# Optimization experiments

Measured on AMD Instinct MI355X. Metric: run time of the kernel, lower is better.

## Reference

```python
import jax, jax.numpy as jnp
import numpy as np

B, N, K, C, CE, H = 2, 2048, 48, 128, 128, 128
IN = 2 * C + CE  # 384
AGG_SCALE = 30.0
LN_EPS = 1e-5


def setup_inputs() -> dict:
    key = jax.random.key(0)
    ks = jax.random.split(key, 12)
    inp = {
        "node_h": jax.random.normal(ks[0], (B, N, C), jnp.float32),
        "edge_h": jax.random.normal(ks[1], (B, N, K, CE), jnp.float32),
        "edge_index": jax.random.randint(ks[2], (B, N, K), 0, N, jnp.int64),
        # message MLP: Linear(IN,H) GELU Linear(H,H) GELU Linear(H,C)
        "W1": jax.random.normal(ks[3], (IN, H), jnp.float32) / np.sqrt(IN),
        "b1": jnp.zeros((H,), jnp.float32),
        "W2": jax.random.normal(ks[4], (H, H), jnp.float32) / np.sqrt(H),
        "b2": jnp.zeros((H,), jnp.float32),
        "W3": jax.random.normal(ks[5], (H, C), jnp.float32) / np.sqrt(H),
        "b3": jnp.zeros((C,), jnp.float32),
        "Wu": jax.random.normal(ks[6], (C, C), jnp.float32) / np.sqrt(C),
        "bu": jnp.zeros((C,), jnp.float32),
        "ln_g": jnp.ones((C,), jnp.float32),
        "ln_b": jnp.zeros((C,), jnp.float32),
    }
    return inp


def _layer_norm(x, g, b):
    mu = jnp.mean(x, axis=-1, keepdims=True)
    var = jnp.var(x, axis=-1, keepdims=True)
    return (x - mu) * jax.lax.rsqrt(var + LN_EPS) * g + b


def _gelu(x):
    return jax.nn.gelu(x, approximate=False)  # torch nn.GELU default (erf)


def reference(node_h, edge_h, edge_index, W1, b1, W2, b2, W3, b3, Wu, bu, ln_g, ln_b):
    b, n, k = edge_index.shape
    c = node_h.shape[-1]
    # gather neighbor node features: (B,N,K,C)
    node_j = jnp.take_along_axis(
        node_h, edge_index.reshape(b, n * k)[..., None], axis=1
    ).reshape(b, n, k, c)
    node_i = jnp.broadcast_to(node_h[:, :, None, :], (b, n, k, c))
    edge_packed = jnp.concatenate([node_i, node_j, edge_h], axis=-1)  # (B,N,K,IN)
    # message MLP
    h = _gelu(edge_packed @ W1 + b1)
    h = _gelu(h @ W2 + b2)
    messages = (h @ W3 + b3).sum(axis=-2) / AGG_SCALE  # (B,N,C)
    # dropout is identity in eval mode
    updated_nodes = _layer_norm(node_h + messages, ln_g, ln_b)
    node_updates = updated_nodes @ Wu + bu
    out = _layer_norm(node_h + node_updates, ln_g, ln_b)
    return out
```

## Files before the change

kernel.cpp:

```cpp
#include <hip/hip_runtime.h>
#include <hip/hip_bf16.h>
#include <math.h>

#define Bn   2
#define Nn   2048
#define Kn   48
#define Cn   128
#define G2   16

#define SIG(r) ((((r) ^ ((r) >> 2))) & 7)

typedef short bf16x8 __attribute__((ext_vector_type(8)));
typedef float f32x4  __attribute__((ext_vector_type(4)));

#if __has_builtin(__builtin_amdgcn_cvt_pk_bf16_f32)
#define HAS_PK 1
#endif

__device__ __forceinline__ short f2bf(float f) {
  union { float f; unsigned u; } v; v.f = f;
  unsigned r = v.u + 0x7fffu + ((v.u >> 16) & 1u);
  return (short)(r >> 16);
}

__device__ __forceinline__ unsigned pk2(float a, float b) {
#ifdef HAS_PK
  auto p = __builtin_amdgcn_cvt_pk_bf16_f32(a, b);
  return __builtin_bit_cast(unsigned, p);
#else
  return (unsigned)(unsigned short)f2bf(a) | ((unsigned)(unsigned short)f2bf(b) << 16);
#endif
}

__device__ __forceinline__ float gelu_f(float x) {
  float z = x * (-2.3021991f - 0.10294200f * x * x);
  float e = __builtin_amdgcn_exp2f(z);
  return x * __builtin_amdgcn_rcpf(1.0f + e);
}

__global__ void pack_weights(const float* __restrict__ W1,
                             const float* __restrict__ W2,
                             const float* __restrict__ W3,
                             const float* __restrict__ Wu,
                             short* __restrict__ ws) {
  int tid = blockIdx.x * blockDim.x + threadIdx.x;
  if (tid >= 192 * 64) return;
  int lane = tid & 63;
  int tile = tid >> 6;
  const float* W; short* dst;
  if (tile < 32)       { W = W1;         dst = ws; }
  else if (tile < 96)  { W = W1 + 16384; dst = ws + 16384; tile -= 32; }
  else if (tile < 128) { W = W2;         dst = ws + 49152; tile -= 96; }
  else if (tile < 160) { W = W3;         dst = ws + 65536; tile -= 128; }
  else                 { W = Wu;         dst = ws + 81920; tile -= 160; }
  int kt = tile >> 3, nt = tile & 7;
  int n  = nt * 16 + (lane & 15);
  int k0 = kt * 32 + (lane >> 4) * 8;
  union { short s[8]; bf16x8 v; } u8;
#pragma unroll
  for (int j = 0; j < 8; j++) u8.s[j] = f2bf(W[(k0 + j) * 128 + n]);
  *reinterpret_cast<bf16x8*>(dst + (tile << 9) + lane * 8) = u8.v;
}

__global__ __launch_bounds__(256, 6)
void node_update_kernel(const float* __restrict__ node_h,
                        const float* __restrict__ edge_h,
                        const int*   __restrict__ edge_index,
                        const short* __restrict__ wpack,
                        const float* __restrict__ b1,
                        const float* __restrict__ b2,
                        float* __restrict__ hs_out) {
  __shared__ __align__(16) char smem[24576];
  short* Xs  = (short*)smem;
  short* H1s = (short*)(smem + 12288);

  const int tid  = threadIdx.x;
  const int blk  = blockIdx.x;
  const int bb   = blk >> 11;
  const int lane = tid & 63;
  const int wave = tid >> 6;
  const int lr   = lane & 15;
  const int lq   = lane >> 4;

  const short* W1i = wpack;
  const short* W1e = wpack + 16384;
  const short* W2p = wpack + 49152;

  const int w  = tid & 31;
  const int rr = tid >> 5;
  int idxv[6];
  if (w < 16) {
#pragma unroll
    for (int k = 0; k < 6; k++)
      idxv[k] = edge_index[blk * Kn + rr + k * 8];
  }

  f32x4 accY[2] = {};
  {
    bf16x8 avk[4] = {{0}, {0}, {0}, {0}};
    if (lr == 0) {
      const float* p = node_h + (size_t)blk * Cn;
#pragma unroll
      for (int kt = 0; kt < 4; kt++) {
        float4 a0 = *reinterpret_cast<const float4*>(p + kt * 32 + lq * 8);
        float4 a1 = *reinterpret_cast<const float4*>(p + kt * 32 + lq * 8 + 4);
        union { unsigned u[4]; bf16x8 v; } q;
        q.u[0] = pk2(a0.x, a0.y); q.u[1] = pk2(a0.z, a0.w);
        q.u[2] = pk2(a1.x, a1.y); q.u[3] = pk2(a1.z, a1.w);
        avk[kt] = q.v;
      }
    }
#pragma unroll
    for (int kt = 0; kt < 4; kt++) {
      bf16x8 bv0 = *reinterpret_cast<const bf16x8*>(W1i + ((kt * 8 + wave * 2 + 0) << 9) + lane * 8);
      bf16x8 bv1 = *reinterpret_cast<const bf16x8*>(W1i + ((kt * 8 + wave * 2 + 1) << 9) + lane * 8);
      accY[0] = __builtin_amdgcn_mfma_f32_16x16x32_bf16(avk[kt], bv0, accY[0], 0, 0, 0);
      accY[1] = __builtin_amdgcn_mfma_f32_16x16x32_bf16(avk[kt], bv1, accY[1], 0, 0, 0);
    }
  }

#pragma unroll
  for (int k = 0; k < 6; k++) {
    int r = rr + k * 8;
    const float* src = (w < 16)
        ? node_h + (size_t)(bb * Nn + idxv[k]) * Cn + w * 8
        : edge_h + ((size_t)blk * Kn + r) * Cn + (w - 16) * 8;
    float4 v0 = *reinterpret_cast<const float4*>(src);
    float4 v1 = *reinterpret_cast<const float4*>(src + 4);
    uint4 p;
    p.x = pk2(v0.x, v0.y); p.y = pk2(v0.z, v0.w);
    p.z = pk2(v1.x, v1.y); p.w = pk2(v1.z, v1.w);
    *reinterpret_cast<uint4*>(&Xs[r * 256 + ((w ^ SIG(r)) << 3)]) = p;
  }
  __syncthreads();

  const int s0 = SIG(lr);
  f32x4 acc[3][2] = {};
#pragma unroll
  for (int kt = 0; kt < 8; kt++) {
    bf16x8 bf0 = *reinterpret_cast<const bf16x8*>(W1e + ((kt * 8 + wave * 2 + 0) << 9) + lane * 8);
    bf16x8 bf1 = *reinterpret_cast<const bf16x8*>(W1e + ((kt * 8 + wave * 2 + 1) << 9) + lane * 8);
    int swA = (((kt * 4 + lq) ^ s0) << 3);
    int swB = swA ^ (4 << 3);
    bf16x8 a0 = *reinterpret_cast<const bf16x8*>(&Xs[(0  + lr) * 256 + swA]);
    bf16x8 a1 = *reinterpret_cast<const bf16x8*>(&Xs[(16 + lr) * 256 + swB]);
    bf16x8 a2 = *reinterpret_cast<const bf16x8*>(&Xs[(32 + lr) * 256 + swA]);
    acc[0][0] = __builtin_amdgcn_mfma_f32_16x16x32_bf16(a0, bf0, acc[0][0], 0, 0, 0);
    acc[0][1] = __builtin_amdgcn_mfma_f32_16x16x32_bf16(a0, bf1, acc[0][1], 0, 0, 0);
    acc[1][0] = __builtin_amdgcn_mfma_f32_16x16x32_bf16(a1, bf0, acc[1][0], 0, 0, 0);
    acc[1][1] = __builtin_amdgcn_mfma_f32_16x16x32_bf16(a1, bf1, acc[1][1], 0, 0, 0);
    acc[2][0] = __builtin_amdgcn_mfma_f32_16x16x32_bf16(a2, bf0, acc[2][0], 0, 0, 0);
    acc[2][1] = __builtin_amdgcn_mfma_f32_16x16x32_bf16(a2, bf1, acc[2][1], 0, 0, 0);
  }
  __syncthreads();

  const int s5 = (lq * 5) & 7;
#pragma unroll
  for (int j = 0; j < 2; j++) {
    int col = (wave * 2 + j) * 16 + lr;
    float yi = __shfl(accY[j][0], lr) + b1[col];
    int cl = col & 7;
#pragma unroll
    for (int mt = 0; mt < 3; mt++) {
      int r0 = mt * 16 + lq * 4;
      int gs = (col >> 3) ^ s5 ^ ((mt & 1) << 2);
      float g0 = gelu_f(acc[mt][j][0] + yi);
      float g1 = gelu_f(acc[mt][j][1] + yi);
      float g2 = gelu_f(acc[mt][j][2] + yi);
      float g3 = gelu_f(acc[mt][j][3] + yi);
      unsigned p01 = pk2(g0, g1), p23 = pk2(g2, g3);
      H1s[(r0 + 0) * 128 + ((gs ^ 0) << 3) + cl] = (short)(p01 & 0xffff);
      H1s[(r0 + 1) * 128 + ((gs ^ 1) << 3) + cl] = (short)(p01 >> 16);
      H1s[(r0 + 2) * 128 + ((gs ^ 2) << 3) + cl] = (short)(p23 & 0xffff);
      H1s[(r0 + 3) * 128 + ((gs ^ 3) << 3) + cl] = (short)(p23 >> 16);
    }
  }
  __syncthreads();

  f32x4 acc2[3][2] = {};
#pragma unroll
  for (int kt = 0; kt < 4; kt++) {
    bf16x8 bf0 = *reinterpret_cast<const bf16x8*>(W2p + ((kt * 8 + wave * 2 + 0) << 9) + lane * 8);
    bf16x8 bf1 = *reinterpret_cast<const bf16x8*>(W2p + ((kt * 8 + wave * 2 + 1) << 9) + lane * 8);
    int swA = (((kt * 4 + lq) ^ s0) << 3);
    int swB = swA ^ (4 << 3);
    bf16x8 a0 = *reinterpret_cast<const bf16x8*>(&H1s[(0  + lr) * 128 + swA]);
    bf16x8 a1 = *reinterpret_cast<const bf16x8*>(&H1s[(16 + lr) * 128 + swB]);
    bf16x8 a2 = *reinterpret_cast<const bf16x8*>(&H1s[(32 + lr) * 128 + swA]);
    acc2[0][0] = __builtin_amdgcn_mfma_f32_16x16x32_bf16(a0, bf0, acc2[0][0], 0, 0, 0);
    acc2[0][1] = __builtin_amdgcn_mfma_f32_16x16x32_bf16(a0, bf1, acc2[0][1], 0, 0, 0);
    acc2[1][0] = __builtin_amdgcn_mfma_f32_16x16x32_bf16(a1, bf0, acc2[1][0], 0, 0, 0);
    acc2[1][1] = __builtin_amdgcn_mfma_f32_16x16x32_bf16(a1, bf1, acc2[1][1], 0, 0, 0);
    acc2[2][0] = __builtin_amdgcn_mfma_f32_16x16x32_bf16(a2, bf0, acc2[2][0], 0, 0, 0);
    acc2[2][1] = __builtin_amdgcn_mfma_f32_16x16x32_bf16(a2, bf1, acc2[2][1], 0, 0, 0);
  }
#pragma unroll
  for (int j = 0; j < 2; j++) {
    int col = (wave * 2 + j) * 16 + lr;
    float bias = b2[col];
    float s = 0.f;
#pragma unroll
    for (int mt = 0; mt < 3; mt++)
#pragma unroll
      for (int r = 0; r < 4; r++) s += gelu_f(acc2[mt][j][r] + bias);
    s += __shfl_xor(s, 16);
    s += __shfl_xor(s, 32);
    if (lq == 0) hs_out[(size_t)blk * Cn + col] = s;
  }
}

__global__ __launch_bounds__(256, 4)
void tail_kernel(const float* __restrict__ node_h,
                 const short* __restrict__ wpack,
                 const float* __restrict__ b3,
                 const float* __restrict__ bu,
                 const float* __restrict__ ln_g,
                 const float* __restrict__ ln_b,
                 float* __restrict__ out) {
  __shared__ __align__(16) char sm2[24832];
  short* hsB = (short*)sm2;
  float* nhr = (float*)(sm2 + 4096);
  float* xs  = (float*)(sm2 + 12288);
  short* usB = (short*)(sm2 + 20736);

  const int tid  = threadIdx.x;
  const int lane = tid & 63;
  const int wave = tid >> 6;
  const int lr   = lane & 15;
  const int lq   = lane >> 4;
  const int n0   = blockIdx.x * G2;

  const short* W3p = wpack + 65536;
  const short* Wup = wpack + 81920;

  {
    int row = tid >> 4, seg = tid & 15;
    const float* p = node_h + (size_t)(n0 + row) * Cn + seg * 8;
    float4 a0 = *reinterpret_cast<const float4*>(p);
    float4 a1 = *reinterpret_cast<const float4*>(p + 4);
    *reinterpret_cast<float4*>(&nhr[row * 128 + seg * 8])     = a0;
    *reinterpret_cast<float4*>(&nhr[row * 128 + seg * 8 + 4]) = a1;
    const float* q = out + (size_t)(n0 + row) * Cn + seg * 8;
    float4 c0 = *reinterpret_cast<const float4*>(q);
    float4 c1 = *reinterpret_cast<const float4*>(q + 4);
    uint4 pk;
    pk.x = pk2(c0.x, c0.y); pk.y = pk2(c0.z, c0.w);
    pk.z = pk2(c1.x, c1.y); pk.w = pk2(c1.z, c1.w);
    *reinterpret_cast<uint4*>(&hsB[row * 128 + ((seg ^ (row & 7)) << 3)]) = pk;
  }
  __syncthreads();

  f32x4 am[2] = {};
#pragma unroll
  for (int kt = 0; kt < 4; kt++) {
    bf16x8 av = *reinterpret_cast<const bf16x8*>(&hsB[lr * 128 + (((kt * 4 + lq) ^ (lr & 7)) << 3)]);
    bf16x8 bv0 = *reinterpret_cast<const bf16x8*>(W3p + ((kt * 8 + wave * 2 + 0) << 9) + lane * 8);
    bf16x8 bv1 = *reinterpret_cast<const bf16x8*>(W3p + ((kt * 8 + wave * 2 + 1) << 9) + lane * 8);
    am[0] = __builtin_amdgcn_mfma_f32_16x16x32_bf16(av, bv0, am[0], 0, 0, 0);
    am[1] = __builtin_amdgcn_mfma_f32_16x16x32_bf16(av, bv1, am[1], 0, 0, 0);
  }
#pragma unroll
  for (int j = 0; j < 2; j++) {
    int col = (wave * 2 + j) * 16 + lr;
    float bb = 48.0f * b3[col];
#pragma unroll
    for (int r = 0; r < 4; r++) {
      int row = lq * 4 + r;
      xs[row * 132 + col] = nhr[row * 128 + col] + (am[j][r] + bb) * (1.0f / 30.0f);
    }
  }
  __syncthreads();

  const float lg1 = ln_g[lane],      lb1v = ln_b[lane];
  const float lg2 = ln_g[lane + 64], lb2v = ln_b[lane + 64];
#pragma unroll
  for (int s = 0; s < 4; s++) {
    int row = wave * 4 + s;
    float v1 = xs[row * 132 + lane];
    float v2 = xs[row * 132 + lane + 64];
    float s1 = v1 + v2, s2 = v1 * v1 + v2 * v2;
#pragma unroll
    for (int off = 32; off >= 1; off >>= 1) {
      s1 += __shfl_xor(s1, off);
      s2 += __shfl_xor(s2, off);
    }
    float mu = s1 * (1.f / 128.f);
    float var = s2 * (1.f / 128.f) - mu * mu;
    float rstd = rsqrtf(var + 1e-5f);
    unsigned u12 = pk2((v1 - mu) * rstd * lg1 + lb1v,
                       (v2 - mu) * rstd * lg2 + lb2v);
    int sw = (row & 7);
    usB[row * 128 + (((lane >> 3) ^ sw) << 3) + (lane & 7)]       = (short)(u12 & 0xffff);
    usB[row * 128 + ((((lane >> 3) + 8) ^ sw) << 3) + (lane & 7)] = (short)(u12 >> 16);
  }
  __syncthreads();

  f32x4 au[2] = {};
#pragma unroll
  for (int kt = 0; kt < 4; kt++) {
    bf16x8 av = *reinterpret_cast<const bf16x8*>(&usB[lr * 128 + (((kt * 4 + lq) ^ (lr & 7)) << 3)]);
    bf16x8 bv0 = *reinterpret_cast<const bf16x8*>(Wup + ((kt * 8 + wave * 2 + 0) << 9) + lane * 8);
    bf16x8 bv1 = *reinterpret_cast<const bf16x8*>(Wup + ((kt * 8 + wave * 2 + 1) << 9) + lane * 8);
    au[0] = __builtin_amdgcn_mfma_f32_16x16x32_bf16(av, bv0, au[0], 0, 0, 0);
    au[1] = __builtin_amdgcn_mfma_f32_16x16x32_bf16(av, bv1, au[1], 0, 0, 0);
  }
  __syncthreads();
#pragma unroll
  for (int j = 0; j < 2; j++) {
    int col = (wave * 2 + j) * 16 + lr;
    float bb = bu[col];
#pragma unroll
    for (int r = 0; r < 4; r++) {
      int row = lq * 4 + r;
      xs[row * 132 + col] = nhr[row * 128 + col] + au[j][r] + bb;
    }
  }
  __syncthreads();

#pragma unroll
  for (int s = 0; s < 4; s++) {
    int row = wave * 4 + s;
    float v1 = xs[row * 132 + lane];
    float v2 = xs[row * 132 + lane + 64];
    float s1 = v1 + v2, s2 = v1 * v1 + v2 * v2;
#pragma unroll
    for (int off = 32; off >= 1; off >>= 1) {
      s1 += __shfl_xor(s1, off);
      s2 += __shfl_xor(s2, off);
    }
    float mu = s1 * (1.f / 128.f);
    float var = s2 * (1.f / 128.f) - mu * mu;
    float rstd = rsqrtf(var + 1e-5f);
    out[(size_t)(n0 + row) * Cn + lane]      = (v1 - mu) * rstd * lg1 + lb1v;
    out[(size_t)(n0 + row) * Cn + lane + 64] = (v2 - mu) * rstd * lg2 + lb2v;
  }
}

extern "C" void kernel_launch(void* const* d_in, const int* in_sizes, int n_in,
                              void* d_out, int out_size, void* d_ws, size_t ws_size,
                              hipStream_t stream) {
  const float* node_h     = (const float*)d_in[0];
  const float* edge_h     = (const float*)d_in[1];
  const int*   edge_index = (const int*)  d_in[2];
  const float* W1 = (const float*)d_in[3];
  const float* b1 = (const float*)d_in[4];
  const float* W2 = (const float*)d_in[5];
  const float* b2 = (const float*)d_in[6];
  const float* W3 = (const float*)d_in[7];
  const float* b3 = (const float*)d_in[8];
  const float* Wu = (const float*)d_in[9];
  const float* bu = (const float*)d_in[10];
  const float* ln_g = (const float*)d_in[11];
  const float* ln_b = (const float*)d_in[12];
  float* out   = (float*)d_out;
  short* wpack = (short*)d_ws;

  pack_weights<<<48, 256, 0, stream>>>(W1, W2, W3, Wu, wpack);
  node_update_kernel<<<Bn * Nn, 256, 0, stream>>>(
      node_h, edge_h, edge_index, wpack, b1, b2, out);
  tail_kernel<<<(Bn * Nn) / G2, 256, 0, stream>>>(
      node_h, wpack, b3, bu, ln_g, ln_b, out);
}
```

Before: 208.5 us.

## Process two nodes per block in node update kernel to amortize weight loads

Each block of the node update kernel now handles two nodes (96 edge rows) rather than one, so every packed weight fragment loaded from global memory feeds twice as many MFMAs. The edge indices and the self-node features are staged in shared memory first. The X buffer and the first-layer hidden buffer now share one larger shared region, and launch bounds drop from 6 to 3 blocks per CU. In exchange there are more accumulator registers per thread, fewer resident waves to hide gather latency, and half as many blocks in the grid.

```diff
diff --git a/kernel.cpp b/kernel.cpp
--- a/kernel.cpp
+++ b/kernel.cpp
@@ -6,6 +6,7 @@
 #define Nn   2048
 #define Kn   48
 #define Cn   128
+#define NB   2
 #define G2   16
 
 #define SIG(r) ((((r) ^ ((r) >> 2))) & 7)
@@ -62,7 +63,7 @@
   *reinterpret_cast<bf16x8*>(dst + (tile << 9) + lane * 8) = u8.v;
 }
 
-__global__ __launch_bounds__(256, 6)
+__global__ __launch_bounds__(256, 3)
 void node_update_kernel(const float* __restrict__ node_h,
                         const float* __restrict__ edge_h,
                         const int*   __restrict__ edge_index,
@@ -70,13 +71,16 @@
                         const float* __restrict__ b1,
                         const float* __restrict__ b2,
                         float* __restrict__ hs_out) {
-  __shared__ __align__(16) char smem[24576];
-  short* Xs  = (short*)smem;
-  short* H1s = (short*)(smem + 12288);
+  __shared__ __align__(16) char smem[50048];
+  short* Xs    = (short*)smem;
+  short* H1s   = (short*)smem;
+  short* nhb   = (short*)(smem + 49152);
+  int*   idx_s = (int*)  (smem + 49664);
 
   const int tid  = threadIdx.x;
-  const int blk  = blockIdx.x;
-  const int bb   = blk >> 11;
+  const int blk2 = blockIdx.x;
+  const int n0   = blk2 * NB;
+  const int bb   = blk2 >> 10;
   const int lane = tid & 63;
   const int wave = tid >> 6;
   const int lr   = lane & 15;
@@ -86,71 +90,55 @@
   const short* W1e = wpack + 16384;
   const short* W2p = wpack + 49152;
 
-  const int w  = tid & 31;
-  const int rr = tid >> 5;
-  int idxv[6];
-  if (w < 16) {
-#pragma unroll
-    for (int k = 0; k < 6; k++)
-      idxv[k] = edge_index[blk * Kn + rr + k * 8];
+  nhb[tid] = f2bf(node_h[(size_t)n0 * Cn + tid]);
+  if (tid < 96) idx_s[tid] = edge_index[blk2 * (NB * Kn) + tid];
+  __syncthreads();
+
+  {
+    const int w  = tid & 31;
+    const int rr = tid >> 5;
+#pragma unroll
+    for (int k = 0; k < 12; k++) {
+      int r = rr + k * 8;
+      const float* src = (w < 16)
+          ? node_h + (size_t)(bb * Nn + idx_s[r]) * Cn + w * 8
+          : edge_h + (size_t)(blk2 * (NB * Kn) + r) * Cn + (w - 16) * 8;
+      float4 v0 = *reinterpret_cast<const float4*>(src);
+      float4 v1 = *reinterpret_cast<const float4*>(src + 4);
+      uint4 p;
+      p.x = pk2(v0.x, v0.y); p.y = pk2(v0.z, v0.w);
+      p.z = pk2(v1.x, v1.y); p.w = pk2(v1.z, v1.w);
+      *reinterpret_cast<uint4*>(&Xs[r * 256 + ((w ^ SIG(r)) << 3)]) = p;
+    }
   }
 
   f32x4 accY[2] = {};
-  {
-    bf16x8 avk[4] = {{0}, {0}, {0}, {0}};
-    if (lr == 0) {
-      const float* p = node_h + (size_t)blk * Cn;
-#pragma unroll
-      for (int kt = 0; kt < 4; kt++) {
-        float4 a0 = *reinterpret_cast<const float4*>(p + kt * 32 + lq * 8);
-        float4 a1 = *reinterpret_cast<const float4*>(p + kt * 32 + lq * 8 + 4);
-        union { unsigned u[4]; bf16x8 v; } q;
-        q.u[0] = pk2(a0.x, a0.y); q.u[1] = pk2(a0.z, a0.w);
-        q.u[2] = pk2(a1.x, a1.y); q.u[3] = pk2(a1.z, a1.w);
-        avk[kt] = q.v;
-      }
-    }
-#pragma unroll
-    for (int kt = 0; kt < 4; kt++) {
-      bf16x8 bv0 = *reinterpret_cast<const bf16x8*>(W1i + ((kt * 8 + wave * 2 + 0) << 9) + lane * 8);
-      bf16x8 bv1 = *reinterpret_cast<const bf16x8*>(W1i + ((kt * 8 + wave * 2 + 1) << 9) + lane * 8);
-      accY[0] = __builtin_amdgcn_mfma_f32_16x16x32_bf16(avk[kt], bv0, accY[0], 0, 0, 0);
-      accY[1] = __builtin_amdgcn_mfma_f32_16x16x32_bf16(avk[kt], bv1, accY[1], 0, 0, 0);
-    }
-  }
-
-#pragma unroll
-  for (int k = 0; k < 6; k++) {
-    int r = rr + k * 8;
-    const float* src = (w < 16)
-        ? node_h + (size_t)(bb * Nn + idxv[k]) * Cn + w * 8
-        : edge_h + ((size_t)blk * Kn + r) * Cn + (w - 16) * 8;
-    float4 v0 = *reinterpret_cast<const float4*>(src);
-    float4 v1 = *reinterpret_cast<const float4*>(src + 4);
-    uint4 p;
-    p.x = pk2(v0.x, v0.y); p.y = pk2(v0.z, v0.w);
-    p.z = pk2(v1.x, v1.y); p.w = pk2(v1.z, v1.w);
-    *reinterpret_cast<uint4*>(&Xs[r * 256 + ((w ^ SIG(r)) << 3)]) = p;
+#pragma unroll
+  for (int kt = 0; kt < 4; kt++) {
+    bf16x8 av = {};
+    if (lr < 2) av = *reinterpret_cast<const bf16x8*>(&nhb[lr * 128 + kt * 32 + lq * 8]);
+    bf16x8 bv0 = *reinterpret_cast<const bf16x8*>(W1i + ((kt * 8 + wave * 2 + 0) << 9) + lane * 8);
+    bf16x8 bv1 = *reinterpret_cast<const bf16x8*>(W1i + ((kt * 8 + wave * 2 + 1) << 9) + lane * 8);
+    accY[0] = __builtin_amdgcn_mfma_f32_16x16x32_bf16(av, bv0, accY[0], 0, 0, 0);
+    accY[1] = __builtin_amdgcn_mfma_f32_16x16x32_bf16(av, bv1, accY[1], 0, 0, 0);
   }
   __syncthreads();
 
   const int s0 = SIG(lr);
-  f32x4 acc[3][2] = {};
+  f32x4 acc[6][2] = {};
 #pragma unroll
   for (int kt = 0; kt < 8; kt++) {
     bf16x8 bf0 = *reinterpret_cast<const bf16x8*>(W1e + ((kt * 8 + wave * 2 + 0) << 9) + lane * 8);
     bf16x8 bf1 = *reinterpret_cast<const bf16x8*>(W1e + ((kt * 8 + wave * 2 + 1) << 9) + lane * 8);
     int swA = (((kt * 4 + lq) ^ s0) << 3);
     int swB = swA ^ (4 << 3);
-    bf16x8 a0 = *reinterpret_cast<const bf16x8*>(&Xs[(0  + lr) * 256 + swA]);
-    bf16x8 a1 = *reinterpret_cast<const bf16x8*>(&Xs[(16 + lr) * 256 + swB]);
-    bf16x8 a2 = *reinterpret_cast<const bf16x8*>(&Xs[(32 + lr) * 256 + swA]);
-    acc[0][0] = __builtin_amdgcn_mfma_f32_16x16x32_bf16(a0, bf0, acc[0][0], 0, 0, 0);
-    acc[0][1] = __builtin_amdgcn_mfma_f32_16x16x32_bf16(a0, bf1, acc[0][1], 0, 0, 0);
-    acc[1][0] = __builtin_amdgcn_mfma_f32_16x16x32_bf16(a1, bf0, acc[1][0], 0, 0, 0);
-    acc[1][1] = __builtin_amdgcn_mfma_f32_16x16x32_bf16(a1, bf1, acc[1][1], 0, 0, 0);
-    acc[2][0] = __builtin_amdgcn_mfma_f32_16x16x32_bf16(a2, bf0, acc[2][0], 0, 0, 0);
-    acc[2][1] = __builtin_amdgcn_mfma_f32_16x16x32_bf16(a2, bf1, acc[2][1], 0, 0, 0);
+#pragma unroll
+    for (int mt = 0; mt < 6; mt++) {
+      bf16x8 a = *reinterpret_cast<const bf16x8*>(
+          &Xs[(mt * 16 + lr) * 256 + ((mt & 1) ? swB : swA)]);
+      acc[mt][0] = __builtin_amdgcn_mfma_f32_16x16x32_bf16(a, bf0, acc[mt][0], 0, 0, 0);
+      acc[mt][1] = __builtin_amdgcn_mfma_f32_16x16x32_bf16(a, bf1, acc[mt][1], 0, 0, 0);
+    }
   }
   __syncthreads();
 
@@ -158,10 +146,12 @@
 #pragma unroll
   for (int j = 0; j < 2; j++) {
     int col = (wave * 2 + j) * 16 + lr;
-    float yi = __shfl(accY[j][0], lr) + b1[col];
+    float yiA = __shfl(accY[j][0], lr) + b1[col];
+    float yiB = __shfl(accY[j][1], lr) + b1[col];
     int cl = col & 7;
 #pragma unroll
-    for (int mt = 0; mt < 3; mt++) {
+    for (int mt = 0; mt < 6; mt++) {
+      float yi = (mt < 3) ? yiA : yiB;
       int r0 = mt * 16 + lq * 4;
       int gs = (col >> 3) ^ s5 ^ ((mt & 1) << 2);
       float g0 = gelu_f(acc[mt][j][0] + yi);
@@ -177,35 +167,40 @@
   }
   __syncthreads();
 
-  f32x4 acc2[3][2] = {};
+  f32x4 acc2[6][2] = {};
 #pragma unroll
   for (int kt = 0; kt < 4; kt++) {
     bf16x8 bf0 = *reinterpret_cast<const bf16x8*>(W2p + ((kt * 8 + wave * 2 + 0) << 9) + lane * 8);
     bf16x8 bf1 = *reinterpret_cast<const bf16x8*>(W2p + ((kt * 8 + wave * 2 + 1) << 9) + lane * 8);
     int swA = (((kt * 4 + lq) ^ s0) << 3);
     int swB = swA ^ (4 << 3);
-    bf16x8 a0 = *reinterpret_cast<const bf16x8*>(&H1s[(0  + lr) * 128 + swA]);
-    bf16x8 a1 = *reinterpret_cast<const bf16x8*>(&H1s[(16 + lr) * 128 + swB]);
-    bf16x8 a2 = *reinterpret_cast<const bf16x8*>(&H1s[(32 + lr) * 128 + swA]);
-    acc2[0][0] = __builtin_amdgcn_mfma_f32_16x16x32_bf16(a0, bf0, acc2[0][0], 0, 0, 0);
-    acc2[0][1] = __builtin_amdgcn_mfma_f32_16x16x32_bf16(a0, bf1, acc2[0][1], 0, 0, 0);
-    acc2[1][0] = __builtin_amdgcn_mfma_f32_16x16x32_bf16(a1, bf0, acc2[1][0], 0, 0, 0);
-    acc2[1][1] = __builtin_amdgcn_mfma_f32_16x16x32_bf16(a1, bf1, acc2[1][1], 0, 0, 0);
-    acc2[2][0] = __builtin_amdgcn_mfma_f32_16x16x32_bf16(a2, bf0, acc2[2][0], 0, 0, 0);
-    acc2[2][1] = __builtin_amdgcn_mfma_f32_16x16x32_bf16(a2, bf1, acc2[2][1], 0, 0, 0);
+#pragma unroll
+    for (int mt = 0; mt < 6; mt++) {
+      bf16x8 a = *reinterpret_cast<const bf16x8*>(
+          &H1s[(mt * 16 + lr) * 128 + ((mt & 1) ? swB : swA)]);
+      acc2[mt][0] = __builtin_amdgcn_mfma_f32_16x16x32_bf16(a, bf0, acc2[mt][0], 0, 0, 0);
+      acc2[mt][1] = __builtin_amdgcn_mfma_f32_16x16x32_bf16(a, bf1, acc2[mt][1], 0, 0, 0);
+    }
   }
 #pragma unroll
   for (int j = 0; j < 2; j++) {
     int col = (wave * 2 + j) * 16 + lr;
     float bias = b2[col];
-    float s = 0.f;
+    float sA = 0.f, sB = 0.f;
 #pragma unroll
     for (int mt = 0; mt < 3; mt++)
 #pragma unroll
-      for (int r = 0; r < 4; r++) s += gelu_f(acc2[mt][j][r] + bias);
-    s += __shfl_xor(s, 16);
-    s += __shfl_xor(s, 32);
-    if (lq == 0) hs_out[(size_t)blk * Cn + col] = s;
+      for (int r = 0; r < 4; r++) sA += gelu_f(acc2[mt][j][r] + bias);
+#pragma unroll
+    for (int mt = 3; mt < 6; mt++)
+#pragma unroll
+      for (int r = 0; r < 4; r++) sB += gelu_f(acc2[mt][j][r] + bias);
+    sA += __shfl_xor(sA, 16); sA += __shfl_xor(sA, 32);
+    sB += __shfl_xor(sB, 16); sB += __shfl_xor(sB, 32);
+    if (lq == 0) {
+      hs_out[(size_t)n0 * Cn + col]       = sA;
+      hs_out[(size_t)(n0 + 1) * Cn + col] = sB;
+    }
   }
 }
 
@@ -356,7 +351,7 @@
   short* wpack = (short*)d_ws;
 
   pack_weights<<<48, 256, 0, stream>>>(W1, W2, W3, Wu, wpack);
-  node_update_kernel<<<Bn * Nn, 256, 0, stream>>>(
+  node_update_kernel<<<(Bn * Nn) / NB, 256, 0, stream>>>(
       node_h, edge_h, edge_index, wpack, b1, b2, out);
   tail_kernel<<<(Bn * Nn) / G2, 256, 0, stream>>>(
       node_h, wpack, b3, bu, ln_g, ln_b, out);
```

After: 212.3 us. About the same (+1.8%).
